# Performance work log

Measured on AMD Instinct MI355X. Metric: run time of the kernel, lower is better.

Reference implementation:

```python
import jax, jax.numpy as jnp
import numpy as np

NUM_GRAPHS = 4096


def setup_inputs() -> dict:
    key = jax.random.key(0)
    ks = jax.random.split(key, 8)
    N, S, V, T = 200000, 128, 64, 64
    d_in, d_mid = S + V + 2 * T, (S + V + 2 * T) // 2
    h = jax.random.normal(ks[0], (N, S), dtype=jnp.float32)
    v = jax.random.normal(ks[1], (N, V, 3), dtype=jnp.float32)
    t = jax.random.normal(ks[2], (N, T, 3, 3), dtype=jnp.float32)
    local_frames = jax.random.normal(ks[3], (N, 3, 3), dtype=jnp.float32)
    batch = jnp.sort(jax.random.randint(ks[4], (N,), 0, NUM_GRAPHS, dtype=jnp.int64))
    # Xavier-uniform linear weights, zero biases (init_weights)
    lim1 = float(np.sqrt(6.0 / (d_in + d_mid)))
    lim2 = float(np.sqrt(6.0 / (d_mid + T)))
    W1 = jax.random.uniform(ks[5], (d_in, d_mid), jnp.float32, -lim1, lim1)
    b1 = jnp.zeros((d_mid,), jnp.float32)
    W2 = jax.random.uniform(ks[6], (d_mid, T), jnp.float32, -lim2, lim2)
    b2 = jnp.zeros((T,), jnp.float32)
    return {"h": h, "v": v, "t": t, "local_frames": local_frames,
            "batch": batch, "W1": W1, "b1": b1, "W2": W2, "b2": b2}


def reference(h, v, t, local_frames, batch, W1, b1, W2, b2):
    N = h.shape[0]
    # rotation-invariant norms
    v_norm = jnp.linalg.norm(v, axis=-1)                       # [N, V]
    trace = jnp.trace(t, axis1=-2, axis2=-1)                   # [N, T]
    frob = jnp.sqrt(jnp.sum(t * t, axis=(-2, -1)))             # [N, T]
    t_inv = jnp.stack([trace, frob], axis=-1).reshape(N, -1)   # [N, 2T]
    norms = jnp.concatenate([h, v_norm, t_inv], axis=-1)       # [N, S+V+2T]
    # gate MLP: Linear -> SiLU -> Linear
    alphas = jax.nn.silu(norms @ W1 + b1) @ W2 + b2            # [N, T]
    # gated channel readout: sum_c alpha_c * T_c
    t_local = jnp.einsum('nc,ncij->nij', alphas, t)            # [N, 3, 3]
    # symmetrize
    t_local = 0.5 * (t_local + jnp.swapaxes(t_local, -1, -2))
    # rotate to global frame: R @ T @ R^T
    t_glob = jnp.einsum('nab,nbc,ndc->nad', local_frames, t_local, local_frames)
    # global add pool over graphs
    t_flat = t_glob.reshape(N, 9)
    pooled = jax.ops.segment_sum(t_flat, batch, num_segments=NUM_GRAPHS)
    return pooled.reshape(-1, 3, 3)
```

## Files before the change

kernel.cpp:

```cpp
#include <hip/hip_runtime.h>
#include <math.h>

typedef __bf16 bf16x8_t __attribute__((ext_vector_type(8)));
typedef unsigned short u16x8_t __attribute__((ext_vector_type(8)));
typedef float f32x4_t __attribute__((ext_vector_type(4)));
typedef float f32x4u __attribute__((ext_vector_type(4), aligned(4)));
typedef float f32x2u __attribute__((ext_vector_type(2), aligned(4)));

#define NB_TOTAL 200000
#define W1P_ELEMS 51200
#define W2P_ELEMS 10240

__device__ __forceinline__ unsigned short f2bf(float f) {
    unsigned int u = __builtin_bit_cast(unsigned int, f);
    u += 0x7fffu + ((u >> 16) & 1u);
    return (unsigned short)(u >> 16);
}

__device__ __forceinline__ int fsoff(int n, int k) {
    return n * 320 + ((((k >> 3) ^ (n & 7)) << 3) | (k & 7));
}

__global__ void kzero(float* __restrict__ out, int n) {
    int i = blockIdx.x * 256 + threadIdx.x;
    if (i < n) out[i] = 0.0f;
}

__global__ void krepack(const float* __restrict__ W1, const float* __restrict__ W2,
                        const int* __restrict__ batch, int nb,
                        unsigned short* __restrict__ w1p, unsigned short* __restrict__ w2p,
                        int* __restrict__ flagp) {
    int tid = blockIdx.x * 256 + threadIdx.x;
    if (tid == 0) *flagp = (batch[nb - 1] == 0) ? 1 : 0;
    if (tid < W1P_ELEMS) {
        int e = tid & 7, L = (tid >> 3) & 63, q = tid >> 9;
        int kt = q % 10, j = q / 10;
        int krow = kt * 32 + (L >> 4) * 8 + e;
        int col  = j * 16 + (L & 15);
        w1p[tid] = f2bf(W1[krow * 160 + col]);
    } else if (tid < W1P_ELEMS + W2P_ELEMS) {
        int s = tid - W1P_ELEMS;
        int e = s & 7, L = (s >> 3) & 63, q = s >> 9;
        int kt = q % 5, j = q / 5;
        int krow = kt * 32 + (L >> 4) * 8 + e;
        int col  = j * 16 + (L & 15);
        w2p[s] = f2bf(W2[krow * 64 + col]);
    }
}

__launch_bounds__(256, 4)
__global__ void kmega(const float* __restrict__ hA, const float* __restrict__ vA,
                      const float* __restrict__ tA, const float* __restrict__ lfA,
                      const int* __restrict__ batch,
                      const float* __restrict__ b1, const float* __restrict__ b2,
                      const unsigned short* __restrict__ w1p,
                      const unsigned short* __restrict__ w2p,
                      const int* __restrict__ flagp,
                      float* __restrict__ out)
{
    __shared__ __align__(16) unsigned char smem[40960];
    unsigned short* Fs = (unsigned short*)smem;
    unsigned short* Hs = (unsigned short*)smem;
    float* alph = (float*)smem;

    const int tid  = threadIdx.x;
    const int w    = tid >> 6;
    const int L    = tid & 63;
    const int quad = L >> 4;
    const int c16  = L & 15;
    const long gbase = (long)blockIdx.x * 64;

    #pragma unroll 4
    for (int i = 0; i < 16; ++i) {
        const int  n = w * 16 + i;
        const long g = gbase + n;
        const float* tp = tA + g * 576 + 9 * L;
        const f32x4u t04 = *(const f32x4u*)tp;
        const f32x4u t48 = *(const f32x4u*)(tp + 4);
        const float  e8  = tp[8];
        const float* vp = vA + g * 192 + 3 * L;
        const f32x2u v01 = *(const f32x2u*)vp;
        const float  v2  = vp[2];
        const f32x2u h2 = *(const f32x2u*)(hA + g * 128 + 2 * L);
        unsigned hp = (unsigned)f2bf(h2.x) | ((unsigned)f2bf(h2.y) << 16);
        *(unsigned*)(Fs + fsoff(n, 2 * L)) = hp;
        Fs[fsoff(n, 128 + L)] = f2bf(sqrtf(v01.x * v01.x + v01.y * v01.y + v2 * v2));
        float tr = t04.x + t48.x + e8;
        float fr = sqrtf(t04.x*t04.x + t04.y*t04.y + t04.z*t04.z + t04.w*t04.w +
                         t48.x*t48.x + t48.y*t48.y + t48.z*t48.z + t48.w*t48.w + e8*e8);
        unsigned tp2 = (unsigned)f2bf(tr) | ((unsigned)f2bf(fr) << 16);
        *(unsigned*)(Fs + fsoff(n, 192 + 2 * L)) = tp2;
    }

    bf16x8_t afrag[10];
    {
        const int row = w * 16 + c16;
        const unsigned short* base = Fs + row * 320;
        const int sw = row & 7;
        #pragma unroll
        for (int kt = 0; kt < 10; ++kt) {
            const int c = kt * 4 + quad;
            afrag[kt] = __builtin_bit_cast(bf16x8_t, *(const u16x8_t*)(base + ((c ^ sw) << 3)));
        }
    }
    __syncthreads();

    {
        const u16x8_t* W1f = (const u16x8_t*)w1p;
        for (int j = 0; j < 10; ++j) {
            f32x4_t acc = {0.f, 0.f, 0.f, 0.f};
            #pragma unroll
            for (int kt = 0; kt < 10; ++kt) {
                bf16x8_t bfrag = __builtin_bit_cast(bf16x8_t, W1f[(j * 10 + kt) * 64 + L]);
                acc = __builtin_amdgcn_mfma_f32_16x16x32_bf16(afrag[kt], bfrag, acc, 0, 0, 0);
            }
            const float bias = b1[j * 16 + c16];
            #pragma unroll
            for (int r = 0; r < 4; ++r) {
                float x = acc[r] + bias;
                float sv = x / (1.0f + __expf(-x));
                Hs[(w * 16 + quad * 4 + r) * 168 + j * 16 + c16] = f2bf(sv);
            }
        }
    }

    bf16x8_t a2[5];
    {
        const unsigned short* hrow = Hs + (w * 16 + c16) * 168;
        #pragma unroll
        for (int kt = 0; kt < 5; ++kt)
            a2[kt] = __builtin_bit_cast(bf16x8_t, *(const u16x8_t*)(hrow + kt * 32 + quad * 8));
    }
    __syncthreads();

    {
        const u16x8_t* W2f = (const u16x8_t*)w2p;
        #pragma unroll
        for (int j = 0; j < 4; ++j) {
            f32x4_t acc = {0.f, 0.f, 0.f, 0.f};
            #pragma unroll
            for (int kt = 0; kt < 5; ++kt) {
                bf16x8_t bfrag = __builtin_bit_cast(bf16x8_t, W2f[(j * 5 + kt) * 64 + L]);
                acc = __builtin_amdgcn_mfma_f32_16x16x32_bf16(a2[kt], bfrag, acc, 0, 0, 0);
            }
            const float bias = b2[j * 16 + c16];
            #pragma unroll
            for (int r = 0; r < 4; ++r)
                alph[(w * 16 + quad * 4 + r) * 68 + j * 16 + c16] = acc[r] + bias;
        }
    }

    const int is64 = *flagp;
    #pragma unroll 4
    for (int i = 0; i < 16; ++i) {
        const int  n = w * 16 + i;
        const long g = gbase + n;
        const float* tp = tA + g * 576 + 9 * L;
        const f32x4u t04 = *(const f32x4u*)tp;
        const f32x4u t48 = *(const f32x4u*)(tp + 4);
        const float  e8  = tp[8];
        const float alpha = alph[n * 68 + L];
        float p0 = alpha * t04.x;
        float p1 = alpha * t48.x;
        float p2 = alpha * e8;
        float p3 = alpha * 0.5f * (t04.y + t04.w);
        float p4 = alpha * 0.5f * (t04.z + t48.z);
        float p5 = alpha * 0.5f * (t48.y + t48.w);
        #pragma unroll
        for (int off = 32; off >= 1; off >>= 1) {
            p0 += __shfl_xor(p0, off, 64);
            p1 += __shfl_xor(p1, off, 64);
            p2 += __shfl_xor(p2, off, 64);
            p3 += __shfl_xor(p3, off, 64);
            p4 += __shfl_xor(p4, off, 64);
            p5 += __shfl_xor(p5, off, 64);
        }
        if (L < 9) {
            const float* Rp = lfA + g * 9;
            const int r = L / 3, c = L % 3;
            float Ra0 = Rp[3*r], Ra1 = Rp[3*r+1], Ra2 = Rp[3*r+2];
            float Rb0 = Rp[3*c], Rb1 = Rp[3*c+1], Rb2 = Rp[3*c+2];
            float u0 = p0*Rb0 + p3*Rb1 + p4*Rb2;
            float u1 = p3*Rb0 + p1*Rb1 + p5*Rb2;
            float u2 = p4*Rb0 + p5*Rb1 + p2*Rb2;
            float val = Ra0*u0 + Ra1*u1 + Ra2*u2;
            const int gi = (int)g;
            const int bg = is64 ? batch[2 * gi] : batch[gi];
            atomicAdd(out + (long)bg * 9 + L, val);
        }
    }
}

extern "C" void kernel_launch(void* const* d_in, const int* in_sizes, int n_in,
                              void* d_out, int out_size, void* d_ws, size_t ws_size,
                              hipStream_t stream)
{
    (void)n_in; (void)ws_size;
    const float* hA  = (const float*)d_in[0];
    const float* vA  = (const float*)d_in[1];
    const float* tA  = (const float*)d_in[2];
    const float* lfA = (const float*)d_in[3];
    const int*   bt  = (const int*)d_in[4];
    const float* W1  = (const float*)d_in[5];
    const float* b1  = (const float*)d_in[6];
    const float* W2  = (const float*)d_in[7];
    const float* b2  = (const float*)d_in[8];
    float* out = (float*)d_out;

    unsigned short* w1p = (unsigned short*)d_ws;
    unsigned short* w2p = (unsigned short*)((char*)d_ws + 102400);
    int* flagp = (int*)((char*)d_ws + 122880);

    kzero<<<(out_size + 255) / 256, 256, 0, stream>>>(out, out_size);
    krepack<<<240, 256, 0, stream>>>(W1, W2, bt, in_sizes[4], w1p, w2p, flagp);
    kmega<<<NB_TOTAL / 64, 256, 0, stream>>>(hA, vA, tA, lfA, bt, b1, b2, w1p, w2p, flagp, out);
}
```

Baseline: 855.2 us.

## Build MFMA A-fragments directly from global memory, dropping shared feature staging

Each lane now loads its own row's h, v and t slices straight from global memory with vector loads and computes the norms and invariants in registers, packing them into bf16 MFMA A-fragments. This removes the shared-memory feature buffer, its writes and reads, and one barrier. Shared memory shrinks to about 21 KB and launch bounds rise to 6 blocks per CU for more occupancy. Per-lane loads become strided across rows rather than coalesced across lanes, and register pressure grows from the large temporary arrays.

```diff
diff --git a/kernel.cpp b/kernel.cpp
--- a/kernel.cpp
+++ b/kernel.cpp
@@ -17,8 +17,11 @@
     return (unsigned short)(u >> 16);
 }
 
-__device__ __forceinline__ int fsoff(int n, int k) {
-    return n * 320 + ((((k >> 3) ^ (n & 7)) << 3) | (k & 7));
+__device__ __forceinline__ bf16x8_t pack8(const float* x) {
+    u16x8_t u;
+    #pragma unroll
+    for (int i = 0; i < 8; ++i) u[i] = f2bf(x[i]);
+    return __builtin_bit_cast(bf16x8_t, u);
 }
 
 __global__ void kzero(float* __restrict__ out, int n) {
@@ -48,7 +51,7 @@
     }
 }
 
-__launch_bounds__(256, 4)
+__launch_bounds__(256, 6)
 __global__ void kmega(const float* __restrict__ hA, const float* __restrict__ vA,
                       const float* __restrict__ tA, const float* __restrict__ lfA,
                       const int* __restrict__ batch,
@@ -58,8 +61,7 @@
                       const int* __restrict__ flagp,
                       float* __restrict__ out)
 {
-    __shared__ __align__(16) unsigned char smem[40960];
-    unsigned short* Fs = (unsigned short*)smem;
+    __shared__ __align__(16) unsigned char smem[21504];
     unsigned short* Hs = (unsigned short*)smem;
     float* alph = (float*)smem;
 
@@ -69,41 +71,53 @@
     const int quad = L >> 4;
     const int c16  = L & 15;
     const long gbase = (long)blockIdx.x * 64;
-
-    #pragma unroll 4
-    for (int i = 0; i < 16; ++i) {
-        const int  n = w * 16 + i;
-        const long g = gbase + n;
-        const float* tp = tA + g * 576 + 9 * L;
-        const f32x4u t04 = *(const f32x4u*)tp;
-        const f32x4u t48 = *(const f32x4u*)(tp + 4);
-        const float  e8  = tp[8];
-        const float* vp = vA + g * 192 + 3 * L;
-        const f32x2u v01 = *(const f32x2u*)vp;
-        const float  v2  = vp[2];
-        const f32x2u h2 = *(const f32x2u*)(hA + g * 128 + 2 * L);
-        unsigned hp = (unsigned)f2bf(h2.x) | ((unsigned)f2bf(h2.y) << 16);
-        *(unsigned*)(Fs + fsoff(n, 2 * L)) = hp;
-        Fs[fsoff(n, 128 + L)] = f2bf(sqrtf(v01.x * v01.x + v01.y * v01.y + v2 * v2));
-        float tr = t04.x + t48.x + e8;
-        float fr = sqrtf(t04.x*t04.x + t04.y*t04.y + t04.z*t04.z + t04.w*t04.w +
-                         t48.x*t48.x + t48.y*t48.y + t48.z*t48.z + t48.w*t48.w + e8*e8);
-        unsigned tp2 = (unsigned)f2bf(tr) | ((unsigned)f2bf(fr) << 16);
-        *(unsigned*)(Fs + fsoff(n, 192 + 2 * L)) = tp2;
-    }
+    const long gm    = gbase + w * 16 + c16;
 
     bf16x8_t afrag[10];
     {
-        const int row = w * 16 + c16;
-        const unsigned short* base = Fs + row * 320;
-        const int sw = row & 7;
-        #pragma unroll
-        for (int kt = 0; kt < 10; ++kt) {
-            const int c = kt * 4 + quad;
-            afrag[kt] = __builtin_bit_cast(bf16x8_t, *(const u16x8_t*)(base + ((c ^ sw) << 3)));
-        }
-    }
-    __syncthreads();
+        const float* hp = hA + gm * 128 + quad * 8;
+        #pragma unroll
+        for (int kt = 0; kt < 4; ++kt) {
+            float x[8];
+            *(f32x4u*)(x)     = *(const f32x4u*)(hp + kt * 32);
+            *(f32x4u*)(x + 4) = *(const f32x4u*)(hp + kt * 32 + 4);
+            afrag[kt] = pack8(x);
+        }
+    }
+    {
+        const float* vp = vA + gm * 192 + quad * 24;
+        #pragma unroll
+        for (int kt2 = 0; kt2 < 2; ++kt2) {
+            float x[24];
+            #pragma unroll
+            for (int q = 0; q < 6; ++q)
+                *(f32x4u*)(x + 4 * q) = *(const f32x4u*)(vp + kt2 * 96 + 4 * q);
+            float nm[8];
+            #pragma unroll
+            for (int c = 0; c < 8; ++c)
+                nm[c] = sqrtf(x[3*c]*x[3*c] + x[3*c+1]*x[3*c+1] + x[3*c+2]*x[3*c+2]);
+            afrag[4 + kt2] = pack8(nm);
+        }
+    }
+    {
+        const float* tp = tA + gm * 576 + quad * 36;
+        #pragma unroll
+        for (int kt4 = 0; kt4 < 4; ++kt4) {
+            float x[36];
+            #pragma unroll
+            for (int q = 0; q < 9; ++q)
+                *(f32x4u*)(x + 4 * q) = *(const f32x4u*)(tp + kt4 * 144 + 4 * q);
+            float ti[8];
+            #pragma unroll
+            for (int c = 0; c < 4; ++c) {
+                const float* b = x + 9 * c;
+                ti[2*c]   = b[0] + b[4] + b[8];
+                ti[2*c+1] = sqrtf(b[0]*b[0] + b[1]*b[1] + b[2]*b[2] + b[3]*b[3] + b[4]*b[4] +
+                                  b[5]*b[5] + b[6]*b[6] + b[7]*b[7] + b[8]*b[8]);
+            }
+            afrag[6 + kt4] = pack8(ti);
+        }
+    }
 
     {
         const u16x8_t* W1f = (const u16x8_t*)w1p;
@@ -117,8 +131,8 @@
             const float bias = b1[j * 16 + c16];
             #pragma unroll
             for (int r = 0; r < 4; ++r) {
-                float x = acc[r] + bias;
-                float sv = x / (1.0f + __expf(-x));
+                float xx = acc[r] + bias;
+                float sv = xx / (1.0f + __expf(-xx));
                 Hs[(w * 16 + quad * 4 + r) * 168 + j * 16 + c16] = f2bf(sv);
             }
         }
```

After: 939.5 us. 9.9% more time.
